# Performance work log

Measured on AMD Instinct MI355X. Metric: run time of the kernel, lower is better.

Reference implementation:

```python
import jax, jax.numpy as jnp
import numpy as np

HS = 4096
NIN = 17   # RFSIZE*RFSIZE + ADDINPUT + NBACTIONS = 9 + 4 + 4
NACT = 4


def setup_inputs() -> dict:
    key = jax.random.key(0)
    ks = jax.random.split(key, 10)
    return {
        "inputs": jax.random.normal(ks[0], (1, NIN), jnp.float32),
        "hidden": jax.random.normal(ks[1], (1, HS), jnp.float32) * 0.1,
        "hebb": jnp.zeros((HS, HS), jnp.float32),
        "et": jnp.zeros((HS, HS), jnp.float32),
        "pw": jnp.zeros((HS, HS), jnp.float32),
        # i2h Linear(17 -> hs)
        "i2h_w": jax.random.normal(ks[2], (HS, NIN), jnp.float32) * (1.0 / np.sqrt(NIN)),
        "i2h_b": jax.random.normal(ks[3], (HS,), jnp.float32) * 0.01,
        # plastic recurrent params: 0.01 * rand, eta = 0.01 * ones(1)
        "w": 0.01 * jax.random.uniform(ks[4], (HS, HS), jnp.float32),
        "alpha": 0.01 * jax.random.uniform(ks[5], (HS, HS), jnp.float32),
        "eta": 0.01 * jnp.ones((1,), jnp.float32),
        # output heads
        "h2o_w": jax.random.normal(ks[6], (NACT, HS), jnp.float32) * (1.0 / np.sqrt(HS)),
        "h2o_b": jax.random.normal(ks[7], (NACT,), jnp.float32) * 0.01,
        "h2v_w": jax.random.normal(ks[8], (1, HS), jnp.float32) * (1.0 / np.sqrt(HS)),
        "h2v_b": jax.random.normal(ks[9], (1,), jnp.float32) * 0.01,
    }


def reference(inputs, hidden, hebb, et, pw,
              i2h_w, i2h_b, w, alpha, eta,
              h2o_w, h2o_b, h2v_w, h2v_b):
    # type='plastic', rule='hebb', clp=0, addpw=0
    # hactiv = tanh(i2h(inputs) + hidden @ (w + alpha * hebb))
    pre = inputs @ i2h_w.T + i2h_b + hidden @ (w + alpha * hebb)  # [1, HS]
    hactiv = jnp.tanh(pre)
    activout = hactiv @ h2o_w.T + h2o_b   # [1, NBACTIONS]
    valueout = hactiv @ h2v_w.T + h2v_b   # [1, 1]
    # deltahebb = outer(hidden[0], hactiv[0])  (batch 1, matches torch.bmm(...)[0])
    deltahebb = hidden[0][:, None] * hactiv[0][None, :]  # [HS, HS]
    hebb_new = (1.0 - eta) * hebb + eta * deltahebb       # eta shape (1,) broadcasts
    # hidden <- hactiv; et, pw untouched for this type
    return activout, valueout, hactiv, hebb_new, et, pw
```

## Files before the change

kernel.cpp:

```cpp
#include <hip/hip_runtime.h>
#include <math.h>

#define HS 4096
#define NIN 17
#define ROW_CHUNKS 512
#define ROWS_PER_CHUNK (HS / ROW_CHUNKS)

typedef float vfloat4  __attribute__((ext_vector_type(4)));
typedef float vfloat4u __attribute__((ext_vector_type(4), aligned(4)));

__device__ __forceinline__ vfloat4 ntload4(const vfloat4* p) {
  return __builtin_nontemporal_load(p);
}
__device__ __forceinline__ void ntstore4u(vfloat4u* p, vfloat4 v) {
  __builtin_nontemporal_store((vfloat4u)v, p);
}

__global__ __launch_bounds__(256) void matvec_k(
    const float* __restrict__ hidden, const float* __restrict__ w,
    const float* __restrict__ alpha, const float* __restrict__ hebb,
    float* __restrict__ partial) {
  const int j4 = blockIdx.x * blockDim.x + threadIdx.x;
  const int row0 = blockIdx.y * ROWS_PER_CHUNK;
  const size_t base = (size_t)row0 * (HS / 4) + j4;
  const vfloat4* wp = reinterpret_cast<const vfloat4*>(w) + base;
  const vfloat4* ap = reinterpret_cast<const vfloat4*>(alpha) + base;
  const vfloat4* bp = reinterpret_cast<const vfloat4*>(hebb) + base;

  vfloat4 wv[ROWS_PER_CHUNK], av[ROWS_PER_CHUNK], bv[ROWS_PER_CHUNK];
#pragma unroll
  for (int r = 0; r < ROWS_PER_CHUNK; ++r) {
    wv[r] = ntload4(wp + (size_t)r * (HS / 4));
    av[r] = ntload4(ap + (size_t)r * (HS / 4));
    bv[r] = bp[(size_t)r * (HS / 4)];
  }

  vfloat4 acc = (vfloat4)(0.f);
#pragma unroll
  for (int r = 0; r < ROWS_PER_CHUNK; ++r) {
    const float h = hidden[row0 + r];
#pragma unroll
    for (int c = 0; c < 4; ++c)
      acc[c] = fmaf(h, fmaf(av[r][c], bv[r][c], wv[r][c]), acc[c]);
  }
  reinterpret_cast<vfloat4*>(partial)[(size_t)blockIdx.y * (HS / 4) + j4] = acc;
}

__global__ __launch_bounds__(256) void finalize_k(
    const float* __restrict__ partial, const float* __restrict__ inputs,
    const float* __restrict__ i2h_w, const float* __restrict__ i2h_b,
    float* __restrict__ out_hactiv) {
  const int t = threadIdx.x;
  const int col = blockIdx.x * 64 + (t & 63);
  const int g = t >> 6;
  float acc = 0.f;
#pragma unroll 16
  for (int k = 0; k < ROW_CHUNKS / 4; ++k)
    acc += partial[(size_t)(g * (ROW_CHUNKS / 4) + k) * HS + col];

  __shared__ float red[256];
  red[t] = acc;
  __syncthreads();
  if (t < 64) {
    float s = red[t] + red[t + 64] + red[t + 128] + red[t + 192];
#pragma unroll
    for (int l = 0; l < NIN; ++l)
      s = fmaf(inputs[l], i2h_w[(size_t)col * NIN + l], s);
    out_hactiv[col] = tanhf(s + i2h_b[col]);
  }
}

__global__ __launch_bounds__(256) void heads_k(
    const float* __restrict__ hactiv, const float* __restrict__ h2o_w,
    const float* __restrict__ h2o_b, const float* __restrict__ h2v_w,
    const float* __restrict__ h2v_b, float* __restrict__ out) {
  const int r = blockIdx.x;
  const float* wrow = (r < 4) ? (h2o_w + (size_t)r * HS) : h2v_w;
  float s = 0.f;
  for (int j = threadIdx.x; j < HS; j += 256) s = fmaf(hactiv[j], wrow[j], s);
  __shared__ float red[256];
  red[threadIdx.x] = s;
  __syncthreads();
  for (int off = 128; off > 0; off >>= 1) {
    if (threadIdx.x < off) red[threadIdx.x] += red[threadIdx.x + off];
    __syncthreads();
  }
  if (threadIdx.x == 0) out[r] = red[0] + ((r < 4) ? h2o_b[r] : h2v_b[0]);
}

__global__ __launch_bounds__(256) void hebb_stream_k(
    const float* __restrict__ hebb, const float* __restrict__ hidden,
    const float* __restrict__ hactiv, const float* __restrict__ eta,
    const float* __restrict__ et, const float* __restrict__ pw,
    float* __restrict__ out_hebb, float* __restrict__ out_et,
    float* __restrict__ out_pw) {
  const float e = eta[0];
  const float one_m_e = 1.f - e;
  const vfloat4*  hebbp = reinterpret_cast<const vfloat4*>(hebb);
  const vfloat4*  etp   = reinterpret_cast<const vfloat4*>(et);
  const vfloat4*  pwp   = reinterpret_cast<const vfloat4*>(pw);
  const vfloat4u* hap   = reinterpret_cast<const vfloat4u*>(hactiv);
  vfloat4u* oheb = reinterpret_cast<vfloat4u*>(out_hebb);
  vfloat4u* oet  = reinterpret_cast<vfloat4u*>(out_et);
  vfloat4u* opw  = reinterpret_cast<vfloat4u*>(out_pw);

  const size_t u0 = (size_t)blockIdx.x * 2048 + threadIdx.x;
#pragma unroll
  for (int i = 0; i < 8; ++i) {
    const size_t u = u0 + (size_t)i * 256;
    const vfloat4 ev = ntload4(etp + u);
    const vfloat4 pv = ntload4(pwp + u);
    const vfloat4 hb = hebbp[u];
    const float ehi = e * hidden[u >> 10];
    const vfloat4 ha = (vfloat4)hap[u & 1023];
    vfloat4 o;
#pragma unroll
    for (int c = 0; c < 4; ++c) o[c] = fmaf(one_m_e, hb[c], ehi * ha[c]);
    ntstore4u(oet + u, ev);
    ntstore4u(opw + u, pv);
    ntstore4u(oheb + u, o);
  }
}

extern "C" void kernel_launch(void* const* d_in, const int* in_sizes, int n_in,
                              void* d_out, int out_size, void* d_ws, size_t ws_size,
                              hipStream_t stream) {
  const float* inputs = (const float*)d_in[0];
  const float* hidden = (const float*)d_in[1];
  const float* hebb   = (const float*)d_in[2];
  const float* et     = (const float*)d_in[3];
  const float* pw     = (const float*)d_in[4];
  const float* i2h_w  = (const float*)d_in[5];
  const float* i2h_b  = (const float*)d_in[6];
  const float* w      = (const float*)d_in[7];
  const float* alpha  = (const float*)d_in[8];
  const float* eta    = (const float*)d_in[9];
  const float* h2o_w  = (const float*)d_in[10];
  const float* h2o_b  = (const float*)d_in[11];
  const float* h2v_w  = (const float*)d_in[12];
  const float* h2v_b  = (const float*)d_in[13];

  float* out = (float*)d_out;
  const size_t NSQ = (size_t)HS * HS;
  float* out_heads  = out;
  float* out_hactiv = out + 5;
  float* out_hebb   = out + 5 + HS;
  float* out_et     = out_hebb + NSQ;
  float* out_pw     = out_et + NSQ;

  const size_t need = (size_t)ROW_CHUNKS * HS * sizeof(float);
  float* partial = (ws_size >= need) ? (float*)d_ws
                                     : (out_hebb + 3 );

  hipLaunchKernelGGL(matvec_k, dim3(HS / 4 / 256, ROW_CHUNKS), dim3(256),
                     0, stream, hidden, w, alpha, hebb, partial);
  hipLaunchKernelGGL(finalize_k, dim3(HS / 64), dim3(256), 0, stream,
                     partial, inputs, i2h_w, i2h_b, out_hactiv);
  hipLaunchKernelGGL(heads_k, dim3(5), dim3(256), 0, stream,
                     out_hactiv, h2o_w, h2o_b, h2v_w, h2v_b, out_heads);
  hipLaunchKernelGGL(hebb_stream_k, dim3(2048), dim3(256), 0, stream,
                     hebb, hidden, out_hactiv, eta, et, pw,
                     out_hebb, out_et, out_pw);
}
```

Measured before the change: 451.3 us.

## Fuse et copy into matvec, heads into hebb stream, align stores via shuffles

Moves the et passthrough copy into the matvec kernel so it overlaps with the memory-bound matvec, and folds the heads reduction into the hebb/pw streaming kernel to drop one launch. Output stores for the 3-float-offset matrices become aligned 16-byte stores: each thread loads two adjacent source vectors and shuffles them, and a single extra block writes the boundary elements. This costs redundant loads of neighbouring vectors and some edge-handling logic.

```diff
diff --git a/kernel.cpp b/kernel.cpp
--- a/kernel.cpp
+++ b/kernel.cpp
@@ -4,28 +4,36 @@
 #define HS 4096
 #define NIN 17
 #define ROW_CHUNKS 512
-#define ROWS_PER_CHUNK (HS / ROW_CHUNKS)
+#define ROWS_PER_CHUNK 8
+#define NSQ ((size_t)HS * (size_t)HS)
+#define NG4 4194303u
 
-typedef float vfloat4  __attribute__((ext_vector_type(4)));
-typedef float vfloat4u __attribute__((ext_vector_type(4), aligned(4)));
+typedef float vfloat4 __attribute__((ext_vector_type(4)));
 
 __device__ __forceinline__ vfloat4 ntload4(const vfloat4* p) {
   return __builtin_nontemporal_load(p);
 }
-__device__ __forceinline__ void ntstore4u(vfloat4u* p, vfloat4 v) {
-  __builtin_nontemporal_store((vfloat4u)v, p);
+__device__ __forceinline__ void ntstore4(vfloat4* p, vfloat4 v) {
+  __builtin_nontemporal_store(v, p);
+}
+__device__ __forceinline__ vfloat4 shift3(vfloat4 a, vfloat4 b) {
+  return __builtin_shufflevector(a, b, 3, 4, 5, 6);
 }
 
-__global__ __launch_bounds__(256) void matvec_k(
+__global__ __launch_bounds__(256) void matvec_et_k(
     const float* __restrict__ hidden, const float* __restrict__ w,
     const float* __restrict__ alpha, const float* __restrict__ hebb,
+    const float* __restrict__ et, float* __restrict__ out_et3,
     float* __restrict__ partial) {
-  const int j4 = blockIdx.x * blockDim.x + threadIdx.x;
+  const int tid = threadIdx.x;
+  const int j4 = blockIdx.x * 256 + tid;
   const int row0 = blockIdx.y * ROWS_PER_CHUNK;
   const size_t base = (size_t)row0 * (HS / 4) + j4;
   const vfloat4* wp = reinterpret_cast<const vfloat4*>(w) + base;
   const vfloat4* ap = reinterpret_cast<const vfloat4*>(alpha) + base;
   const vfloat4* bp = reinterpret_cast<const vfloat4*>(hebb) + base;
+  const vfloat4* ep = reinterpret_cast<const vfloat4*>(et);
+  vfloat4* oe = reinterpret_cast<vfloat4*>(out_et3);
 
   vfloat4 wv[ROWS_PER_CHUNK], av[ROWS_PER_CHUNK], bv[ROWS_PER_CHUNK];
 #pragma unroll
@@ -33,6 +41,16 @@
     wv[r] = ntload4(wp + (size_t)r * (HS / 4));
     av[r] = ntload4(ap + (size_t)r * (HS / 4));
     bv[r] = bp[(size_t)r * (HS / 4)];
+  }
+
+  const unsigned s0 = (blockIdx.y * 4u + blockIdx.x) * 2048u + tid;
+#pragma unroll
+  for (int m = 0; m < 8; ++m) {
+    const unsigned s = s0 + 256u * m;
+    const unsigned sc = (s < NG4) ? s : (NG4 - 1u);
+    const vfloat4 a = ntload4(ep + sc);
+    const vfloat4 b = ntload4(ep + sc + 1);
+    if (s < NG4) ntstore4(oe + s, shift3(a, b));
   }
 
   vfloat4 acc = (vfloat4)(0.f);
@@ -70,55 +88,73 @@
   }
 }
 
-__global__ __launch_bounds__(256) void heads_k(
-    const float* __restrict__ hactiv, const float* __restrict__ h2o_w,
-    const float* __restrict__ h2o_b, const float* __restrict__ h2v_w,
-    const float* __restrict__ h2v_b, float* __restrict__ out) {
-  const int r = blockIdx.x;
-  const float* wrow = (r < 4) ? (h2o_w + (size_t)r * HS) : h2v_w;
-  float s = 0.f;
-  for (int j = threadIdx.x; j < HS; j += 256) s = fmaf(hactiv[j], wrow[j], s);
-  __shared__ float red[256];
-  red[threadIdx.x] = s;
-  __syncthreads();
-  for (int off = 128; off > 0; off >>= 1) {
-    if (threadIdx.x < off) red[threadIdx.x] += red[threadIdx.x + off];
-    __syncthreads();
-  }
-  if (threadIdx.x == 0) out[r] = red[0] + ((r < 4) ? h2o_b[r] : h2v_b[0]);
-}
-
-__global__ __launch_bounds__(256) void hebb_stream_k(
+__global__ __launch_bounds__(256) void hebb_pw_heads_k(
     const float* __restrict__ hebb, const float* __restrict__ hidden,
     const float* __restrict__ hactiv, const float* __restrict__ eta,
-    const float* __restrict__ et, const float* __restrict__ pw,
+    const float* __restrict__ pw, const float* __restrict__ et,
     float* __restrict__ out_hebb, float* __restrict__ out_et,
-    float* __restrict__ out_pw) {
-  const float e = eta[0];
-  const float one_m_e = 1.f - e;
-  const vfloat4*  hebbp = reinterpret_cast<const vfloat4*>(hebb);
-  const vfloat4*  etp   = reinterpret_cast<const vfloat4*>(et);
-  const vfloat4*  pwp   = reinterpret_cast<const vfloat4*>(pw);
-  const vfloat4u* hap   = reinterpret_cast<const vfloat4u*>(hactiv);
-  vfloat4u* oheb = reinterpret_cast<vfloat4u*>(out_hebb);
-  vfloat4u* oet  = reinterpret_cast<vfloat4u*>(out_et);
-  vfloat4u* opw  = reinterpret_cast<vfloat4u*>(out_pw);
+    float* __restrict__ out_pw,
+    const float* __restrict__ h2o_w, const float* __restrict__ h2o_b,
+    const float* __restrict__ h2v_w, const float* __restrict__ h2v_b,
+    float* __restrict__ out_heads) {
+  const int b = blockIdx.x;
+  if (b >= 2048) {
+    if (b < 2053) {
+      const int r = b - 2048;
+      const float* wrow = (r < 4) ? (h2o_w + (size_t)r * HS) : h2v_w;
+      float s = 0.f;
+      for (int j = threadIdx.x; j < HS; j += 256) s = fmaf(hactiv[j], wrow[j], s);
+      __shared__ float red[256];
+      red[threadIdx.x] = s;
+      __syncthreads();
+      for (int off = 128; off > 0; off >>= 1) {
+        if (threadIdx.x < off) red[threadIdx.x] += red[threadIdx.x + off];
+        __syncthreads();
+      }
+      if (threadIdx.x == 0) out_heads[r] = red[0] + ((r < 4) ? h2o_b[r] : h2v_b[0]);
+    } else if (threadIdx.x == 0) {
+      const float e = eta[0], om = 1.f - e;
+      const float f0 = e * hidden[0], fl = e * hidden[HS - 1];
+#pragma unroll
+      for (int k = 0; k < 3; ++k) {
+        out_et[k] = et[k];
+        out_pw[k] = pw[k];
+        out_hebb[k] = fmaf(om, hebb[k], f0 * hactiv[k]);
+      }
+      out_et[NSQ - 1] = et[NSQ - 1];
+      out_pw[NSQ - 1] = pw[NSQ - 1];
+      out_hebb[NSQ - 1] = fmaf(om, hebb[NSQ - 1], fl * hactiv[HS - 1]);
+    }
+    return;
+  }
 
-  const size_t u0 = (size_t)blockIdx.x * 2048 + threadIdx.x;
+  const float e = eta[0], om = 1.f - e;
+  const vfloat4* hebbp = reinterpret_cast<const vfloat4*>(hebb);
+  const vfloat4* pwp = reinterpret_cast<const vfloat4*>(pw);
+  vfloat4* oheb = reinterpret_cast<vfloat4*>(out_hebb + 3);
+  vfloat4* opw = reinterpret_cast<vfloat4*>(out_pw + 3);
+  const unsigned s0 = b * 2048u + threadIdx.x;
 #pragma unroll
-  for (int i = 0; i < 8; ++i) {
-    const size_t u = u0 + (size_t)i * 256;
-    const vfloat4 ev = ntload4(etp + u);
-    const vfloat4 pv = ntload4(pwp + u);
-    const vfloat4 hb = hebbp[u];
-    const float ehi = e * hidden[u >> 10];
-    const vfloat4 ha = (vfloat4)hap[u & 1023];
-    vfloat4 o;
+  for (int m = 0; m < 8; ++m) {
+    const unsigned s = s0 + 256u * m;
+    const unsigned sc = (s < NG4) ? s : (NG4 - 1u);
+    const vfloat4 pA = ntload4(pwp + sc);
+    const vfloat4 pB = ntload4(pwp + sc + 1);
+    const vfloat4 hA = hebbp[sc];
+    const vfloat4 hB = hebbp[sc + 1];
+    const unsigned rA = sc >> 10, rB = (sc + 1) >> 10;
+    const unsigned cA = (sc & 1023u) * 4u, cB = ((sc + 1) & 1023u) * 4u;
+    const float fA = e * hidden[rA], fB = e * hidden[rB];
+    vfloat4 oA, oB;
 #pragma unroll
-    for (int c = 0; c < 4; ++c) o[c] = fmaf(one_m_e, hb[c], ehi * ha[c]);
-    ntstore4u(oet + u, ev);
-    ntstore4u(opw + u, pv);
-    ntstore4u(oheb + u, o);
+    for (int c = 0; c < 4; ++c) {
+      oA[c] = fmaf(om, hA[c], fA * hactiv[cA + c]);
+      oB[c] = fmaf(om, hB[c], fB * hactiv[cB + c]);
+    }
+    if (s < NG4) {
+      ntstore4(opw + s, shift3(pA, pB));
+      ntstore4(oheb + s, shift3(oA, oB));
+    }
   }
 }
 
@@ -141,7 +177,6 @@
   const float* h2v_b  = (const float*)d_in[13];
 
   float* out = (float*)d_out;
-  const size_t NSQ = (size_t)HS * HS;
   float* out_heads  = out;
   float* out_hactiv = out + 5;
   float* out_hebb   = out + 5 + HS;
@@ -152,13 +187,12 @@
   float* partial = (ws_size >= need) ? (float*)d_ws
                                      : (out_hebb + 3 );
 
-  hipLaunchKernelGGL(matvec_k, dim3(HS / 4 / 256, ROW_CHUNKS), dim3(256),
-                     0, stream, hidden, w, alpha, hebb, partial);
+  hipLaunchKernelGGL(matvec_et_k, dim3(4, ROW_CHUNKS), dim3(256), 0, stream,
+                     hidden, w, alpha, hebb, et, out_et + 3, partial);
   hipLaunchKernelGGL(finalize_k, dim3(HS / 64), dim3(256), 0, stream,
                      partial, inputs, i2h_w, i2h_b, out_hactiv);
-  hipLaunchKernelGGL(heads_k, dim3(5), dim3(256), 0, stream,
-                     out_hactiv, h2o_w, h2o_b, h2v_w, h2v_b, out_heads);
-  hipLaunchKernelGGL(hebb_stream_k, dim3(2048), dim3(256), 0, stream,
-                     hebb, hidden, out_hactiv, eta, et, pw,
-                     out_hebb, out_et, out_pw);
+  hipLaunchKernelGGL(hebb_pw_heads_k, dim3(2054), dim3(256), 0, stream,
+                     hebb, hidden, out_hactiv, eta, pw, et,
+                     out_hebb, out_et, out_pw,
+                     h2o_w, h2o_b, h2v_w, h2v_b, out_heads);
 }
```

New measurement: 451.8 us. About the same (+0.1%).
